# Kernel optimization log

Hardware: AMD Instinct MI355X
Metric: run time of the kernel (lower is better)

Reference implementation:

```python
import jax, jax.numpy as jnp
import numpy as np

CONF_THRES = 0.7
IOU_THRES = 0.45
TOP_K = 1000  # max candidates kept per image after confidence filtering (YOLOv5 max_nms-style cap)
IMG_SIZE = 640.0


def _box_iou(boxes):
    """Pairwise IoU of [K,4] xyxy boxes -> [K,K]."""
    area = (boxes[:, 2] - boxes[:, 0]) * (boxes[:, 3] - boxes[:, 1])
    lt = jnp.maximum(boxes[:, None, :2], boxes[None, :, :2])
    rb = jnp.minimum(boxes[:, None, 2:], boxes[None, :, 2:])
    wh = jnp.clip(rb - lt, 0.0)
    inter = wh[..., 0] * wh[..., 1]
    return inter / (area[:, None] + area[None, :] - inter + 1e-7)


def _nms_single(pred):
    """YOLOv5-style NMS for one image. pred: [N, 9] = xywh, obj, cls_conf, pitch, yaw, roll.
    Returns fixed-shape padded detections [TOP_K, 9] and keep mask [TOP_K]."""
    obj = pred[:, 4]
    conf = obj * pred[:, 5]  # nc=1: conf = obj_conf * cls_conf
    valid = (obj > CONF_THRES) & (conf > CONF_THRES)
    score = jnp.where(valid, conf, -1.0)

    top_scores, idx = jax.lax.top_k(score, TOP_K)
    p = pred[idx]  # [TOP_K, 9]
    xy, wh = p[:, :2], p[:, 2:4]
    boxes = jnp.concatenate([xy - wh * 0.5, xy + wh * 0.5], axis=-1)  # xywh -> xyxy

    keep0 = top_scores > CONF_THRES
    iou = _box_iou(boxes)  # [TOP_K, TOP_K]
    ar = jnp.arange(TOP_K)

    # Greedy NMS: boxes are score-sorted; box j is suppressed if a kept earlier box overlaps > thresh.
    def body(i, keep):
        sup = (iou[i] > IOU_THRES) & (ar > i) & keep[i]
        return keep & (~sup)

    keep = jax.lax.fori_loop(0, TOP_K, body, keep0)

    cls = jnp.zeros((TOP_K, 1), boxes.dtype)  # single class (head)
    out = jnp.concatenate([boxes, top_scores[:, None], cls, p[:, 6:9]], axis=-1)  # [TOP_K, 9]
    out = out * keep[:, None].astype(out.dtype)  # zero padded/suppressed rows
    return out, keep


def setup_inputs() -> dict:
    key = jax.random.key(0)
    B, N = 32, 25200
    r = jax.random.uniform(key, (B, N, 9), dtype=jnp.float32)
    xy = r[..., :2] * IMG_SIZE                 # box centers in pixels
    wh = r[..., 2:4] * 128.0 + 4.0             # box sizes 4..132 px
    obj = r[..., 4:5]                          # objectness in [0,1)
    cls = r[..., 5:6] * 0.5 + 0.5              # class conf in [0.5,1)
    ang = (r[..., 6:9] - 0.5) * 2.0            # normalized pitch/yaw/roll
    prediction = jnp.concatenate([xy, wh, obj, cls, ang], axis=-1)
    return {"prediction": prediction}


def reference(prediction):
    out, keep = jax.vmap(_nms_single)(prediction)
    return out, keep
```

## Files before the change

### kernel.cpp

```cpp
#include <hip/hip_runtime.h>
#include <stdint.h>

#pragma clang fp contract(off)

#define BATCH 32
#define NPRED 25200
#define ROWF 9
#define TOPK 1000
#define SUBS 8
#define ROWS_PER_SUB (NPRED / SUBS)
#define SUBCAP 512
#define CONF_T 0.7f
#define IOU_T 0.45f
#define KW 16
#define SUPROW 1024

typedef unsigned long long u64;
typedef unsigned int u32;

#define WS_CAND 0
#define WS_SUP  (1048576)
#define WS_BX   (WS_SUP + 4194304)
#define WS_AREA (WS_BX + 512000)
#define WS_SA   (WS_AREA + 128000)
#define WS_KW   (WS_SA + 512000)

__device__ __forceinline__ u64 readlane64(u64 v, int l) {
    u32 lo = __builtin_amdgcn_readlane((u32)v, (u32)l);
    u32 hi = __builtin_amdgcn_readlane((u32)(v >> 32), (u32)l);
    return ((u64)hi << 32) | lo;
}

__global__ __launch_bounds__(512) void compact_sort_kernel(const float* __restrict__ pred,
                                                           u64* __restrict__ cand_ws) {
    __shared__ float stage[512 * ROWF];
    __shared__ u64 skey[SUBCAP];
    __shared__ u32 cnt;
    int bs = blockIdx.x;
    int b = bs >> 3, s = bs & 7;
    int tid = threadIdx.x;
    if (tid == 0) cnt = 0;
    skey[tid] = 0;
    __syncthreads();
    int r0 = s * ROWS_PER_SUB;
    for (int c0 = 0; c0 < ROWS_PER_SUB; c0 += 512) {
        int nrows = ROWS_PER_SUB - c0; if (nrows > 512) nrows = 512;
        int nfl = nrows * ROWF;
        size_t g0 = ((size_t)b * NPRED + r0 + c0) * ROWF;
        int h = (int)((4 - (g0 & 3)) & 3); if (h > nfl) h = nfl;
        if (tid < h) stage[tid] = pred[g0 + tid];
        int nv = (nfl - h) >> 2;
        const float4* pv = (const float4*)(pred + g0 + h);
        for (int v = tid; v < nv; v += 512) {
            float4 q = pv[v];
            int d = h + v * 4;
            stage[d] = q.x; stage[d + 1] = q.y; stage[d + 2] = q.z; stage[d + 3] = q.w;
        }
        for (int t2 = h + nv * 4 + tid; t2 < nfl; t2 += 512) stage[t2] = pred[g0 + t2];
        __syncthreads();
        if (tid < nrows) {
            float obj = stage[tid * ROWF + 4];
            float cls = stage[tid * ROWF + 5];
            float conf = obj * cls;
            if (obj > CONF_T && conf > CONF_T) {
                int r = r0 + c0 + tid;
                u32 slot = atomicAdd(&cnt, 1u);
                if (slot < SUBCAP)
                    skey[slot] = ((u64)__float_as_uint(conf) << 32) | (u64)(u32)(~(u32)r);
            }
        }
        __syncthreads();
    }
    for (int k = 2; k <= SUBCAP; k <<= 1) {
        for (int j = k >> 1; j > 0; j >>= 1) {
            int t = tid, p = t ^ j;
            if (p > t) {
                u64 a = skey[t], c2 = skey[p];
                bool desc = ((t & k) == 0);
                if (desc ? (a < c2) : (a > c2)) { skey[t] = c2; skey[p] = a; }
            }
            __syncthreads();
        }
    }
    cand_ws[(size_t)bs * SUBCAP + tid] = skey[tid];
}

__global__ __launch_bounds__(1024) void topk_kernel(const float* __restrict__ pred,
                                                    const u64* __restrict__ cand_ws,
                                                    float4* __restrict__ bx_ws,
                                                    float* __restrict__ area_ws,
                                                    float4* __restrict__ sa_ws,
                                                    u64* __restrict__ kw_ws) {
    __shared__ u64 lists[SUBS * SUBCAP];
    __shared__ u64 tkey[TOPK];
    __shared__ u64 kws[KW];
    int b = blockIdx.x, tid = threadIdx.x;
    for (int t = tid; t < SUBS * SUBCAP; t += 1024)
        lists[t] = cand_ws[(size_t)b * SUBS * SUBCAP + t];
    if (tid < KW) kws[tid] = 0;
    if (tid < TOPK) tkey[tid] = 0;
    __syncthreads();
    for (int k = 0; k < (SUBS * SUBCAP) / 1024; ++k) {
        int g = tid + (k << 10);
        u64 key = lists[g];
        if (!key) continue;
        int lo[SUBS];
#pragma unroll
        for (int l = 0; l < SUBS; ++l) lo[l] = 0;
#pragma unroll
        for (int w2 = SUBCAP; w2 >= 1; w2 >>= 1) {
#pragma unroll
            for (int l = 0; l < SUBS; ++l) {
                int p = lo[l] + w2;
                if (p <= SUBCAP && lists[(l << 9) + p - 1] > key) lo[l] = p;
            }
        }
        int rank = 0;
#pragma unroll
        for (int l = 0; l < SUBS; ++l) rank += lo[l];
        if (rank < TOPK) tkey[rank] = key;
    }
    __syncthreads();
    if (tid < TOPK) {
        u64 key = tkey[tid];
        float4 box = make_float4(0.f, 0.f, 0.f, 0.f);
        float ar = 0.f;
        float4 sa = make_float4(0.f, 0.f, 0.f, 0.f);
        if (key) {
            float sc = __uint_as_float((u32)(key >> 32));
            u32 r = ~(u32)key;
            const float* p = pred + ((size_t)b * NPRED + r) * ROWF;
            float x = p[0], y = p[1], w = p[2], hh = p[3];
            box = make_float4(x - w * 0.5f, y - hh * 0.5f, x + w * 0.5f, y + hh * 0.5f);
            ar = (box.z - box.x) * (box.w - box.y);
            sa = make_float4(sc, p[6], p[7], p[8]);
            atomicOr(&kws[tid >> 6], 1ull << (tid & 63));
        }
        bx_ws[b * TOPK + tid] = box;
        area_ws[b * TOPK + tid] = ar;
        sa_ws[b * TOPK + tid] = sa;
    }
    __syncthreads();
    if (tid < KW) kw_ws[b * KW + tid] = kws[tid];
}

__global__ __launch_bounds__(1024) void supmat_kernel(const float4* __restrict__ bx_ws,
                                                      const float* __restrict__ area_ws,
                                                      u64* __restrict__ sup_g) {
    __shared__ float4 bx_s[TOPK];
    __shared__ float  ar_s[TOPK];
    int b = blockIdx.x >> 3, q = blockIdx.x & 7;
    int tid = threadIdx.x;
    if (tid < TOPK) { bx_s[tid] = bx_ws[b * TOPK + tid]; ar_s[tid] = area_ws[b * TOPK + tid]; }
    __syncthreads();
    int wave = tid >> 6, lane = tid & 63;
    for (int pass = 0; pass < 2; ++pass) {
        int t = (pass == 0) ? (q * 16 + wave) : ((wave == 15) ? 128 + q : 136);
        if (t >= 136) continue;
        int iw = 0, rem = t, c = 16;
        while (rem >= c) { rem -= c; c--; iw++; }
        int jw = iw + rem;
        int i = iw * 64 + lane;
        bool act = i < TOPK;
        float4 bi = act ? bx_s[i] : make_float4(0.f, 0.f, 0.f, 0.f);
        float ai = act ? ar_s[i] : 0.f;
        u64 m = 0;
        int jbase = jw << 6;
        int jend = jbase + 64; if (jend > TOPK) jend = TOPK;
        for (int j = jbase; j < jend; ++j) {
            float4 bj = bx_s[j];
            float aj = ar_s[j];
            float lx = fmaxf(bi.x, bj.x);
            float ly = fmaxf(bi.y, bj.y);
            float rx = fminf(bi.z, bj.z);
            float ry = fminf(bi.w, bj.w);
            float iw2 = rx - lx; iw2 = iw2 > 0.f ? iw2 : 0.f;
            float ih = ry - ly; ih = ih > 0.f ? ih : 0.f;
            float inter = iw2 * ih;
            float den = ai + aj - inter + 1e-7f;
            float iou = inter / den;
            if (act && j > i && iou > IOU_T) m |= 1ull << (j - jbase);
        }
        if (act) sup_g[((size_t)b * KW + jw) * SUPROW + i] = m;
    }
}

__global__ __launch_bounds__(1024) void scan_out_kernel(const u64* __restrict__ sup_g,
                                                        const u64* __restrict__ kw_ws,
                                                        const float4* __restrict__ bx_ws,
                                                        const float4* __restrict__ sa_ws,
                                                        float* __restrict__ out,
                                                        float* __restrict__ keepout) {
    __shared__ u64 keep_lds[KW];
    __shared__ u64 acc_lds;
    int b = blockIdx.x, tid = threadIdx.x;
    int w = tid >> 6, lane = tid & 63;
    const u64* S = sup_g + (size_t)b * KW * SUPROW;

    u64 sup_reg[KW];
    u64 diagreg = 0;
#pragma unroll
    for (int bi = 0; bi < KW; ++bi) {
        sup_reg[bi] = S[(size_t)w * SUPROW + (bi << 6) + lane];
        if (bi == w) diagreg = sup_reg[bi];
    }
    if (tid < KW) keep_lds[tid] = kw_ws[b * KW + tid];
    __syncthreads();

    u64 nzmask = __ballot(diagreg != 0);

#pragma unroll
    for (int bi = 0; bi < KW; ++bi) {
        if (w == bi) {
            u64 cur = keep_lds[bi];
            u64 active = cur & nzmask;
            while (active) {
                int i = __ffsll((long long)active) - 1;
                u64 wi = readlane64(diagreg, i);
                active &= active - 1;
                cur &= ~wi;
                active &= ~wi;
            }
            if (lane == 0) { keep_lds[bi] = cur; acc_lds = cur; }
        }
        __syncthreads();
        if (w > bi) {
            u64 A = acc_lds;
            u64 myv = sup_reg[bi];
            bool accb = (A >> lane) & 1ull;
            u64 lanes = __ballot(accb && myv != 0ull);
            if (lanes) {
                u64 wred = 0;
                while (lanes) {
                    int l = __ffsll((long long)lanes) - 1;
                    wred |= readlane64(myv, l);
                    lanes &= lanes - 1;
                }
                if (lane == 0) keep_lds[w] &= ~wred;
            }
        }
        __syncthreads();
    }

    if (tid < TOPK) {
        bool kp = (keep_lds[tid >> 6] >> (tid & 63)) & 1ull;
        float4 bx = bx_ws[b * TOPK + tid];
        float4 sa = sa_ws[b * TOPK + tid];
        size_t ob = ((size_t)b * TOPK + tid) * ROWF;
        out[ob + 0] = kp ? bx.x : 0.f;
        out[ob + 1] = kp ? bx.y : 0.f;
        out[ob + 2] = kp ? bx.z : 0.f;
        out[ob + 3] = kp ? bx.w : 0.f;
        out[ob + 4] = kp ? sa.x : 0.f;
        out[ob + 5] = 0.f;
        out[ob + 6] = kp ? sa.y : 0.f;
        out[ob + 7] = kp ? sa.z : 0.f;
        out[ob + 8] = kp ? sa.w : 0.f;
        keepout[(size_t)b * TOPK + tid] = kp ? 1.0f : 0.0f;
    }
}

extern "C" void kernel_launch(void* const* d_in, const int* in_sizes, int n_in,
                              void* d_out, int out_size, void* d_ws, size_t ws_size,
                              hipStream_t stream) {
    const float* pred = (const float*)d_in[0];
    float* out = (float*)d_out;
    float* keepout = out + (size_t)BATCH * TOPK * ROWF;
    char* ws = (char*)d_ws;
    u64* cand_ws = (u64*)(ws + WS_CAND);
    u64* sup_g = (u64*)(ws + WS_SUP);
    float4* bx_ws = (float4*)(ws + WS_BX);
    float* area_ws = (float*)(ws + WS_AREA);
    float4* sa_ws = (float4*)(ws + WS_SA);
    u64* kw_ws = (u64*)(ws + WS_KW);

    compact_sort_kernel<<<BATCH * SUBS, 512, 0, stream>>>(pred, cand_ws);
    topk_kernel<<<BATCH, 1024, 0, stream>>>(pred, cand_ws, bx_ws, area_ws, sa_ws, kw_ws);
    supmat_kernel<<<BATCH * 8, 1024, 0, stream>>>(bx_ws, area_ws, sup_g);
    scan_out_kernel<<<BATCH, 1024, 0, stream>>>(sup_g, kw_ws, bx_ws, sa_ws, out, keepout);
}
```

Before: 142.9 us.

## Split top-k ranking across sub-blocks and gather boxes directly from predictions

The single-block-per-image top-k kernel becomes a rank kernel launched over batch×subs blocks, each ranking one sublist's candidates and scattering keys straight to a global top-k key array. Box and area construction moves into the suppression-matrix kernel, and the output kernel re-gathers box and angle data from the original predictions using the keys. This removes the intermediate box, area, score and keep-word buffers and spreads ranking over more blocks. In exchange, each rank block reloads all eight sublists, and predictions are gathered twice.

```diff
diff --git a/kernel.cpp b/kernel.cpp
--- a/kernel.cpp
+++ b/kernel.cpp
@@ -14,16 +14,14 @@
 #define IOU_T 0.45f
 #define KW 16
 #define SUPROW 1024
+#define TKROW 1024
 
 typedef unsigned long long u64;
 typedef unsigned int u32;
 
 #define WS_CAND 0
-#define WS_SUP  (1048576)
-#define WS_BX   (WS_SUP + 4194304)
-#define WS_AREA (WS_BX + 512000)
-#define WS_SA   (WS_AREA + 128000)
-#define WS_KW   (WS_SA + 512000)
+#define WS_TKEY (1048576)
+#define WS_SUP  (WS_TKEY + 262144)
 
 __device__ __forceinline__ u64 readlane64(u64 v, int l) {
     u32 lo = __builtin_amdgcn_readlane((u32)v, (u32)l);
@@ -32,7 +30,8 @@
 }
 
 __global__ __launch_bounds__(512) void compact_sort_kernel(const float* __restrict__ pred,
-                                                           u64* __restrict__ cand_ws) {
+                                                           u64* __restrict__ cand_ws,
+                                                           u64* __restrict__ tkey_ws) {
     __shared__ float stage[512 * ROWF];
     __shared__ u64 skey[SUBCAP];
     __shared__ u32 cnt;
@@ -41,6 +40,7 @@
     int tid = threadIdx.x;
     if (tid == 0) cnt = 0;
     skey[tid] = 0;
+    if (tid < 128) tkey_ws[bs * 128 + tid] = 0;
     __syncthreads();
     int r0 = s * ROWS_PER_SUB;
     for (int c0 = 0; c0 < ROWS_PER_SUB; c0 += 512) {
@@ -85,25 +85,17 @@
     cand_ws[(size_t)bs * SUBCAP + tid] = skey[tid];
 }
 
-__global__ __launch_bounds__(1024) void topk_kernel(const float* __restrict__ pred,
-                                                    const u64* __restrict__ cand_ws,
-                                                    float4* __restrict__ bx_ws,
-                                                    float* __restrict__ area_ws,
-                                                    float4* __restrict__ sa_ws,
-                                                    u64* __restrict__ kw_ws) {
+__global__ __launch_bounds__(512) void rank_kernel(const u64* __restrict__ cand_ws,
+                                                   u64* __restrict__ tkey_ws) {
     __shared__ u64 lists[SUBS * SUBCAP];
-    __shared__ u64 tkey[TOPK];
-    __shared__ u64 kws[KW];
-    int b = blockIdx.x, tid = threadIdx.x;
-    for (int t = tid; t < SUBS * SUBCAP; t += 1024)
-        lists[t] = cand_ws[(size_t)b * SUBS * SUBCAP + t];
-    if (tid < KW) kws[tid] = 0;
-    if (tid < TOPK) tkey[tid] = 0;
-    __syncthreads();
-    for (int k = 0; k < (SUBS * SUBCAP) / 1024; ++k) {
-        int g = tid + (k << 10);
-        u64 key = lists[g];
-        if (!key) continue;
+    int bs = blockIdx.x;
+    int b = bs >> 3, s = bs & 7;
+    int tid = threadIdx.x;
+    const u64* src = cand_ws + (size_t)b * SUBS * SUBCAP;
+    for (int t = tid; t < SUBS * SUBCAP; t += 512) lists[t] = src[t];
+    __syncthreads();
+    u64 key = lists[(s << 9) + tid];
+    if (key) {
         int lo[SUBS];
 #pragma unroll
         for (int l = 0; l < SUBS; ++l) lo[l] = 0;
@@ -118,40 +110,30 @@
         int rank = 0;
 #pragma unroll
         for (int l = 0; l < SUBS; ++l) rank += lo[l];
-        if (rank < TOPK) tkey[rank] = key;
-    }
-    __syncthreads();
+        if (rank < TOPK) tkey_ws[(size_t)b * TKROW + rank] = key;
+    }
+}
+
+__global__ __launch_bounds__(1024) void supmat_kernel(const float* __restrict__ pred,
+                                                      const u64* __restrict__ tkey_ws,
+                                                      u64* __restrict__ sup_g) {
+    __shared__ float4 bx_s[TOPK];
+    __shared__ float  ar_s[TOPK];
+    int b = blockIdx.x >> 3, q = blockIdx.x & 7;
+    int tid = threadIdx.x;
     if (tid < TOPK) {
-        u64 key = tkey[tid];
+        u64 key = tkey_ws[(size_t)b * TKROW + tid];
         float4 box = make_float4(0.f, 0.f, 0.f, 0.f);
         float ar = 0.f;
-        float4 sa = make_float4(0.f, 0.f, 0.f, 0.f);
         if (key) {
-            float sc = __uint_as_float((u32)(key >> 32));
             u32 r = ~(u32)key;
             const float* p = pred + ((size_t)b * NPRED + r) * ROWF;
             float x = p[0], y = p[1], w = p[2], hh = p[3];
             box = make_float4(x - w * 0.5f, y - hh * 0.5f, x + w * 0.5f, y + hh * 0.5f);
             ar = (box.z - box.x) * (box.w - box.y);
-            sa = make_float4(sc, p[6], p[7], p[8]);
-            atomicOr(&kws[tid >> 6], 1ull << (tid & 63));
-        }
-        bx_ws[b * TOPK + tid] = box;
-        area_ws[b * TOPK + tid] = ar;
-        sa_ws[b * TOPK + tid] = sa;
-    }
-    __syncthreads();
-    if (tid < KW) kw_ws[b * KW + tid] = kws[tid];
-}
-
-__global__ __launch_bounds__(1024) void supmat_kernel(const float4* __restrict__ bx_ws,
-                                                      const float* __restrict__ area_ws,
-                                                      u64* __restrict__ sup_g) {
-    __shared__ float4 bx_s[TOPK];
-    __shared__ float  ar_s[TOPK];
-    int b = blockIdx.x >> 3, q = blockIdx.x & 7;
-    int tid = threadIdx.x;
-    if (tid < TOPK) { bx_s[tid] = bx_ws[b * TOPK + tid]; ar_s[tid] = area_ws[b * TOPK + tid]; }
+        }
+        bx_s[tid] = box; ar_s[tid] = ar;
+    }
     __syncthreads();
     int wave = tid >> 6, lane = tid & 63;
     for (int pass = 0; pass < 2; ++pass) {
@@ -185,10 +167,9 @@
     }
 }
 
-__global__ __launch_bounds__(1024) void scan_out_kernel(const u64* __restrict__ sup_g,
-                                                        const u64* __restrict__ kw_ws,
-                                                        const float4* __restrict__ bx_ws,
-                                                        const float4* __restrict__ sa_ws,
+__global__ __launch_bounds__(1024) void scan_out_kernel(const float* __restrict__ pred,
+                                                        const u64* __restrict__ tkey_ws,
+                                                        const u64* __restrict__ sup_g,
                                                         float* __restrict__ out,
                                                         float* __restrict__ keepout) {
     __shared__ u64 keep_lds[KW];
@@ -197,6 +178,10 @@
     int w = tid >> 6, lane = tid & 63;
     const u64* S = sup_g + (size_t)b * KW * SUPROW;
 
+    u64 key = tkey_ws[(size_t)b * TKROW + tid];
+    u64 keep0 = __ballot(key != 0ull);
+    if (lane == 0) keep_lds[w] = keep0;
+
     u64 sup_reg[KW];
     u64 diagreg = 0;
 #pragma unroll
@@ -204,7 +189,6 @@
         sup_reg[bi] = S[(size_t)w * SUPROW + (bi << 6) + lane];
         if (bi == w) diagreg = sup_reg[bi];
     }
-    if (tid < KW) keep_lds[tid] = kw_ws[b * KW + tid];
     __syncthreads();
 
     u64 nzmask = __ballot(diagreg != 0);
@@ -243,19 +227,21 @@
     }
 
     if (tid < TOPK) {
-        bool kp = (keep_lds[tid >> 6] >> (tid & 63)) & 1ull;
-        float4 bx = bx_ws[b * TOPK + tid];
-        float4 sa = sa_ws[b * TOPK + tid];
+        bool kp = ((keep_lds[w] >> lane) & 1ull) != 0;
+        float o0 = 0.f, o1 = 0.f, o2 = 0.f, o3 = 0.f, o4 = 0.f, o6 = 0.f, o7 = 0.f, o8 = 0.f;
+        if (kp) {
+            u32 r = ~(u32)key;
+            const float* p = pred + ((size_t)b * NPRED + r) * ROWF;
+            float x = p[0], y = p[1], wd = p[2], hh = p[3];
+            o0 = x - wd * 0.5f; o1 = y - hh * 0.5f;
+            o2 = x + wd * 0.5f; o3 = y + hh * 0.5f;
+            o4 = __uint_as_float((u32)(key >> 32));
+            o6 = p[6]; o7 = p[7]; o8 = p[8];
+        }
         size_t ob = ((size_t)b * TOPK + tid) * ROWF;
-        out[ob + 0] = kp ? bx.x : 0.f;
-        out[ob + 1] = kp ? bx.y : 0.f;
-        out[ob + 2] = kp ? bx.z : 0.f;
-        out[ob + 3] = kp ? bx.w : 0.f;
-        out[ob + 4] = kp ? sa.x : 0.f;
-        out[ob + 5] = 0.f;
-        out[ob + 6] = kp ? sa.y : 0.f;
-        out[ob + 7] = kp ? sa.z : 0.f;
-        out[ob + 8] = kp ? sa.w : 0.f;
+        out[ob + 0] = o0; out[ob + 1] = o1; out[ob + 2] = o2; out[ob + 3] = o3;
+        out[ob + 4] = o4; out[ob + 5] = 0.f;
+        out[ob + 6] = o6; out[ob + 7] = o7; out[ob + 8] = o8;
         keepout[(size_t)b * TOPK + tid] = kp ? 1.0f : 0.0f;
     }
 }
@@ -268,14 +254,11 @@
     float* keepout = out + (size_t)BATCH * TOPK * ROWF;
     char* ws = (char*)d_ws;
     u64* cand_ws = (u64*)(ws + WS_CAND);
+    u64* tkey_ws = (u64*)(ws + WS_TKEY);
     u64* sup_g = (u64*)(ws + WS_SUP);
-    float4* bx_ws = (float4*)(ws + WS_BX);
-    float* area_ws = (float*)(ws + WS_AREA);
-    float4* sa_ws = (float4*)(ws + WS_SA);
-    u64* kw_ws = (u64*)(ws + WS_KW);
-
-    compact_sort_kernel<<<BATCH * SUBS, 512, 0, stream>>>(pred, cand_ws);
-    topk_kernel<<<BATCH, 1024, 0, stream>>>(pred, cand_ws, bx_ws, area_ws, sa_ws, kw_ws);
-    supmat_kernel<<<BATCH * 8, 1024, 0, stream>>>(bx_ws, area_ws, sup_g);
-    scan_out_kernel<<<BATCH, 1024, 0, stream>>>(sup_g, kw_ws, bx_ws, sa_ws, out, keepout);
-}
+
+    compact_sort_kernel<<<BATCH * SUBS, 512, 0, stream>>>(pred, cand_ws, tkey_ws);
+    rank_kernel<<<BATCH * SUBS, 512, 0, stream>>>(cand_ws, tkey_ws);
+    supmat_kernel<<<BATCH * SUBS, 1024, 0, stream>>>(pred, tkey_ws, sup_g);
+    scan_out_kernel<<<BATCH, 1024, 0, stream>>>(pred, tkey_ws, sup_g, out, keepout);
+}
```

Measured after the change: 131.7 us. 1.09x faster.
